# Optimization experiments

Measured on AMD Instinct MI355X. Metric: run time of the kernel, lower is better.

Reference implementation:

```python
import jax, jax.numpy as jnp
import numpy as np

B, NQ, NKV = 4, 1024, 2048
DQ, DC, DI, H = 1024, 1024, 1024, 16
DH = DI // H
EPS = 1e-5


def layer_norm(x, gamma, beta):
    mu = jnp.mean(x, axis=-1, keepdims=True)
    var = jnp.var(x, axis=-1, keepdims=True)
    return (x - mu) * jax.lax.rsqrt(var + EPS) * gamma + beta


def setup_inputs() -> dict:
    key = jax.random.key(0)
    ks = jax.random.split(key, 6)
    s = 0.02
    return {
        "q": jax.random.normal(ks[0], (B, NQ, DQ), jnp.float32),
        "context": jax.random.normal(ks[1], (B, NKV, DC), jnp.float32),
        "Wq": jax.random.normal(ks[2], (DI, DQ), jnp.float32) * s,
        "Wkv": jax.random.normal(ks[3], (2 * DI, DC), jnp.float32) * s,
        "Wproj": jax.random.normal(ks[4], (DQ, DI), jnp.float32) * s,
        "bproj": jnp.zeros((DQ,), jnp.float32),
        "q_gamma": jnp.ones((DQ,), jnp.float32),
        "q_beta": jnp.zeros((DQ,), jnp.float32),
        "c_gamma": jnp.ones((DC,), jnp.float32),
        "c_beta": jnp.zeros((DC,), jnp.float32),
    }


def reference(q, context, Wq, Wkv, Wproj, bproj, q_gamma, q_beta, c_gamma, c_beta):
    scale = DH ** -0.5
    qn = layer_norm(q, q_gamma, q_beta)            # [b, nq, dq]
    cn = layer_norm(context, c_gamma, c_beta)      # [b, nkv, dc]
    qp = qn @ Wq.T                                  # [b, nq, di]
    kv = cn @ Wkv.T                                 # [b, nkv, 2*di]
    k, v = kv[..., :DI], kv[..., DI:]
    qh = qp.reshape(B, NQ, H, DH)
    kh = k.reshape(B, NKV, H, DH)
    vh = v.reshape(B, NKV, H, DH)
    attn = jnp.einsum('bnhd,bmhd->bhnm', qh, kh) * scale   # [b,h,nq,nkv]
    attn = jax.nn.softmax(attn, axis=-1)
    out = jnp.einsum('bhnm,bmhd->bnhd', attn, vh).reshape(B, NQ, DI)
    return out @ Wproj.T + bproj
```

## Files before the change

kernel.cpp:

```cpp
#include <hip/hip_runtime.h>
#include <hip/hip_bf16.h>
#include <stdint.h>

#define B_N 4
#define NQ 1024
#define NKV 2048
#define DI 1024
#define H 16
#define DH 64

using bf16 = __bf16;
typedef bf16 bf16x8 __attribute__((ext_vector_type(8)));
typedef bf16 bf16x4 __attribute__((ext_vector_type(4)));
typedef float f32x4 __attribute__((ext_vector_type(4)));

typedef const __attribute__((address_space(1))) void* gptr_t;
typedef __attribute__((address_space(3))) void* sptr_t;

__global__ __launch_bounds__(256) void cvt_all(const float* __restrict__ Wq,
    const float* __restrict__ Wkv, const float* __restrict__ Wproj,
    bf16* __restrict__ oq, bf16* __restrict__ okv, bf16* __restrict__ op) {
  int i = blockIdx.x * 256 + threadIdx.x;
  const float* src; bf16* dst; int j;
  if (i < 262144)      { src = Wq;    dst = oq;  j = i; }
  else if (i < 786432) { src = Wkv;   dst = okv; j = i - 262144; }
  else                 { src = Wproj; dst = op;  j = i - 786432; }
  float4 v = reinterpret_cast<const float4*>(src)[j];
  bf16x4 o;
  o[0] = (bf16)v.x; o[1] = (bf16)v.y; o[2] = (bf16)v.z; o[3] = (bf16)v.w;
  reinterpret_cast<bf16x4*>(dst)[j] = o;
}

__global__ __launch_bounds__(256) void ln_kernel(const float* __restrict__ q,
    const float* __restrict__ ctx,
    const float* __restrict__ qg, const float* __restrict__ qb,
    const float* __restrict__ cg, const float* __restrict__ cb,
    bf16* __restrict__ qn, bf16* __restrict__ cn) {
  int row = blockIdx.x;
  const float* x; const float* gamma; const float* beta; bf16* out; int r;
  if (row < 4096) { x = q;   gamma = qg; beta = qb; out = qn; r = row; }
  else            { x = ctx; gamma = cg; beta = cb; out = cn; r = row - 4096; }
  int t = threadIdx.x;
  const float4 v = reinterpret_cast<const float4*>(x + (size_t)r * 1024)[t];
  float s = v.x + v.y + v.z + v.w;
  float s2 = v.x*v.x + v.y*v.y + v.z*v.z + v.w*v.w;
#pragma unroll
  for (int m = 1; m < 64; m <<= 1) { s += __shfl_xor(s, m); s2 += __shfl_xor(s2, m); }
  __shared__ float red[8];
  int wid = t >> 6;
  if ((t & 63) == 0) { red[wid] = s; red[wid + 4] = s2; }
  __syncthreads();
  float ts  = red[0] + red[1] + red[2] + red[3];
  float ts2 = red[4] + red[5] + red[6] + red[7];
  float mean = ts * (1.0f / 1024.0f);
  float var  = ts2 * (1.0f / 1024.0f) - mean * mean;
  float rstd = rsqrtf(var + 1e-5f);
  float4 g  = reinterpret_cast<const float4*>(gamma)[t];
  float4 bb = reinterpret_cast<const float4*>(beta)[t];
  bf16x4 o;
  o[0] = (bf16)((v.x - mean) * rstd * g.x + bb.x);
  o[1] = (bf16)((v.y - mean) * rstd * g.y + bb.y);
  o[2] = (bf16)((v.z - mean) * rstd * g.z + bb.z);
  o[3] = (bf16)((v.w - mean) * rstd * g.w + bb.w);
  reinterpret_cast<bf16x4*>(out + (size_t)r * 1024)[t] = o;
}

template<int MODE, int BN>
__device__ __forceinline__ void gemm_body(bf16* lA, bf16* lB,
    const bf16* __restrict__ A, const bf16* __restrict__ Bm,
    void* __restrict__ out0, void* __restrict__ out1,
    const float* __restrict__ bias, int M, int N, int bid) {
  constexpr int K = 1024;
  constexpr int MI = (BN == 128) ? 4 : 2;
  constexpr int NBL = (BN == 128) ? 4 : 2;
  const int nbn = N / BN;
  const int bm = bid / nbn, bn = bid - bm * nbn;
  const int m0 = bm << 7, n0 = bn * BN;
  const int tid = threadIdx.x;
  const int lane = tid & 63, wid = tid >> 6;
  const int rowb = (BN == 128) ? ((wid >> 1) * 64) : (wid * 32);
  const int colb = (BN == 128) ? ((wid & 1) * 64) : 0;
  const int l15 = lane & 15, lg = lane >> 4;

  f32x4 acc[MI][4] = {};

  const bf16* gA[4]; const bf16* gB[NBL];
#pragma unroll
  for (int u = 0; u < 4; ++u) {
    int s = tid + u * 256;
    int row = s >> 3, c8 = (s & 7) ^ (row & 7);
    gA[u] = A + (size_t)(m0 + row) * K + c8 * 8;
  }
#pragma unroll
  for (int u = 0; u < NBL; ++u) {
    int s = tid + u * 256;
    int row = s >> 3, c8 = (s & 7) ^ (row & 7);
    gB[u] = Bm + (size_t)(n0 + row) * K + c8 * 8;
  }

  const int sw = l15 & 7;

  for (int k0 = 0; k0 < K; k0 += 64) {
#pragma unroll
    for (int u = 0; u < 4; ++u)
      __builtin_amdgcn_global_load_lds((gptr_t)(gA[u] + k0), (sptr_t)(lA + (tid + u * 256) * 8), 16, 0, 0);
#pragma unroll
    for (int u = 0; u < NBL; ++u)
      __builtin_amdgcn_global_load_lds((gptr_t)(gB[u] + k0), (sptr_t)(lB + (tid + u * 256) * 8), 16, 0, 0);
    __syncthreads();
#pragma unroll
    for (int ks2 = 0; ks2 < 2; ++ks2) {
      const int soff = ((ks2 * 4 + lg) ^ sw) * 8;
      bf16x8 af[MI], bfr[4];
#pragma unroll
      for (int i = 0; i < MI; ++i)
        af[i]  = *reinterpret_cast<const bf16x8*>(lA + (rowb + i * 16 + l15) * 64 + soff);
#pragma unroll
      for (int j = 0; j < 4; ++j)
        bfr[j] = *reinterpret_cast<const bf16x8*>(lB + (colb + j * 16 + l15) * 64 + soff);
#pragma unroll
      for (int i = 0; i < MI; ++i)
#pragma unroll
        for (int j = 0; j < 4; ++j)
          acc[i][j] = __builtin_amdgcn_mfma_f32_16x16x32_bf16(af[i], bfr[j], acc[i][j], 0, 0, 0);
    }
    __syncthreads();
  }

  const int mB = m0 + rowb + lg * 4;
  const int nB = n0 + colb + l15;
  if constexpr (MODE == 0) {
    bf16* o = reinterpret_cast<bf16*>(out0);
    constexpr float SC = 0.125f * 1.44269504089f;
#pragma unroll
    for (int i = 0; i < MI; ++i)
#pragma unroll
      for (int j = 0; j < 4; ++j)
#pragma unroll
        for (int r = 0; r < 4; ++r)
          o[(size_t)(mB + i * 16 + r) * N + nB + j * 16] = (bf16)(acc[i][j][r] * SC);
  } else if constexpr (MODE == 2) {
    float* o = reinterpret_cast<float*>(out0);
#pragma unroll
    for (int j = 0; j < 4; ++j) {
      float bj = bias[nB + j * 16];
#pragma unroll
      for (int i = 0; i < MI; ++i)
#pragma unroll
        for (int r = 0; r < 4; ++r)
          o[(size_t)(mB + i * 16 + r) * N + nB + j * 16] = acc[i][j][r] + bj;
    }
  } else {
    if (n0 < 1024) {
      bf16* o = reinterpret_cast<bf16*>(out0);
#pragma unroll
      for (int i = 0; i < MI; ++i)
#pragma unroll
        for (int j = 0; j < 4; ++j)
#pragma unroll
          for (int r = 0; r < 4; ++r)
            o[(size_t)(mB + i * 16 + r) * 1024 + nB + j * 16] = (bf16)acc[i][j][r];
    } else {
      bf16* o = reinterpret_cast<bf16*>(out1);
#pragma unroll
      for (int i = 0; i < MI; ++i) {
        int m = mB + i * 16;
        int bb_ = m >> 11, kv = m & 2047;
        int u = kv & 63;
        int c = (u & 32) | ((u & 12) << 1) | ((u & 16) >> 2) | (u & 3);
        int col = (kv & ~63) | c;
#pragma unroll
        for (int j = 0; j < 4; ++j) {
          int nv = nB + j * 16 - 1024;
          bf16x4 pk;
          pk[0] = (bf16)acc[i][j][0]; pk[1] = (bf16)acc[i][j][1];
          pk[2] = (bf16)acc[i][j][2]; pk[3] = (bf16)acc[i][j][3];
          *reinterpret_cast<bf16x4*>(o + ((size_t)(bb_ << 10) + nv) * 2048 + col) = pk;
        }
      }
    }
  }
}

template<int MODE, int BN>
__global__ __launch_bounds__(256) void gemm_bt(const bf16* __restrict__ A,
    const bf16* __restrict__ Bm, void* __restrict__ out0, void* __restrict__ out1,
    const float* __restrict__ bias, int M, int N) {
  __shared__ bf16 lA[128 * 64];
  __shared__ bf16 lB[BN * 64];
  const int cpx = gridDim.x >> 3;
  const int bid = (blockIdx.x & 7) * cpx + (blockIdx.x >> 3);
  gemm_body<MODE, BN>(lA, lB, A, Bm, out0, out1, bias, M, N, bid);
}

__global__ __launch_bounds__(256) void gemm_fused(
    const bf16* __restrict__ qn, const bf16* __restrict__ Wq, void* __restrict__ qpb,
    const bf16* __restrict__ cn, const bf16* __restrict__ Wkv,
    void* __restrict__ kbuf, void* __restrict__ vT) {
  __shared__ bf16 lA[128 * 64];
  __shared__ bf16 lB[128 * 64];
  if (blockIdx.x < 1024) {
    int rb = blockIdx.x;
    int bid = (rb & 7) * 128 + (rb >> 3);
    gemm_body<1, 128>(lA, lB, cn, Wkv, kbuf, vT, nullptr, 8192, 2048, bid);
  } else {
    int rb = blockIdx.x - 1024;
    int bid = (rb & 7) * 32 + (rb >> 3);
    gemm_body<0, 128>(lA, lB, qn, Wq, qpb, nullptr, nullptr, 4096, 1024, bid);
  }
}

__global__ __launch_bounds__(512, 4) void attn_kernel(const bf16* __restrict__ qp,
    const bf16* __restrict__ kk, const bf16* __restrict__ vTp, bf16* __restrict__ out) {
  __shared__ bf16 smem[32768];
  const int pos = blockIdx.x;
  const int idx = pos >> 3;
  const int bh = ((idx >> 3) << 3) | (pos & 7);
  const int qt = idx & 7;
  const int b = bh >> 4, h = bh & 15;
  const int tid = threadIdx.x;
  const int lane = tid & 63, w = tid >> 6;
  const int l15 = lane & 15, lg = lane >> 4;

  const bf16* Qb = qp + (size_t)(b * NQ + qt * 128 + w * 16) * DI + h * DH;
  const bf16* Kb = kk + (size_t)b * NKV * DI + h * DH;
  const bf16* Vb = vTp + (size_t)(b * DI + h * DH) * NKV;

  const int sA = tid, sB = tid + 512;
  const int rKA = ((sA >> 7) << 4) | (sA & 15), cKA = ((sA >> 4) & 7) * 8;
  const int rKB = ((sB >> 7) << 4) | (sB & 15), cKB = ((sB >> 4) & 7) * 8;
  const int rVA = ((sA >> 8) << 4) | (sA & 15), cVA = ((sA >> 6) & 3) * 32 + ((sA >> 4) & 3) * 8;
  const int rVB = ((sB >> 8) << 4) | (sB & 15), cVB = ((sB >> 6) & 3) * 32 + ((sB >> 4) & 3) * 8;
  const bf16* pKA = Kb + (size_t)rKA * DI + cKA;
  const bf16* pKB = Kb + (size_t)rKB * DI + cKB;
  const bf16* pVA = Vb + (size_t)rVA * NKV + cVA;
  const bf16* pVB = Vb + (size_t)rVB * NKV + cVB;

#define STAGE_KV(bufsel, kv)                                                                        \
  do {                                                                                              \
    __builtin_amdgcn_global_load_lds((gptr_t)(pKA + (size_t)(kv) * DI),                             \
                                     (sptr_t)(smem + (bufsel) * 8192 + sA * 8), 16, 0, 0);          \
    __builtin_amdgcn_global_load_lds((gptr_t)(pKB + (size_t)(kv) * DI),                             \
                                     (sptr_t)(smem + (bufsel) * 8192 + sB * 8), 16, 0, 0);          \
    __builtin_amdgcn_global_load_lds((gptr_t)(pVA + (kv)),                                          \
                                     (sptr_t)(smem + 16384 + (bufsel) * 8192 + sA * 8), 16, 0, 0);  \
    __builtin_amdgcn_global_load_lds((gptr_t)(pVB + (kv)),                                          \
                                     (sptr_t)(smem + 16384 + (bufsel) * 8192 + sB * 8), 16, 0, 0);  \
  } while (0)

  bf16x8 qf[2];
#pragma unroll
  for (int ks = 0; ks < 2; ++ks)
    qf[ks] = *reinterpret_cast<const bf16x8*>(Qb + (size_t)l15 * DI + ks * 32 + lg * 8);

  f32x4 o[4] = {};
  float mrun = -1e30f;
  float lpart = 0.0f;

  STAGE_KV(0, 0);
  __syncthreads();
  int cur = 0;

  for (int kv0 = 0; kv0 < NKV; kv0 += 128) {
    const bool notlast = (kv0 + 128 < NKV);
    if (notlast) STAGE_KV(cur ^ 1, kv0 + 128);

    const bf16* Kl = smem + cur * 8192;
    const bf16* Vl = smem + 16384 + cur * 8192;

    f32x4 s[8] = {};
#pragma unroll
    for (int h2 = 0; h2 < 2; ++h2) {
      bf16x8 kf[4][2];
#pragma unroll
      for (int ni = 0; ni < 4; ++ni)
#pragma unroll
        for (int ks = 0; ks < 2; ++ks)
          kf[ni][ks] = *reinterpret_cast<const bf16x8*>(Kl + (((h2 * 4 + ni) * 2 + ks) * 64 + lane) * 8);
      __builtin_amdgcn_s_setprio(1);
#pragma unroll
      for (int ni = 0; ni < 4; ++ni)
#pragma unroll
        for (int ks = 0; ks < 2; ++ks)
          s[h2 * 4 + ni] = __builtin_amdgcn_mfma_f32_16x16x32_bf16(kf[ni][ks], qf[ks], s[h2 * 4 + ni], 0, 0, 0);
      __builtin_amdgcn_s_setprio(0);
    }

    f32x4 mv = s[0];
#pragma unroll
    for (int i = 1; i < 8; ++i) {
      mv[0] = fmaxf(mv[0], s[i][0]); mv[1] = fmaxf(mv[1], s[i][1]);
      mv[2] = fmaxf(mv[2], s[i][2]); mv[3] = fmaxf(mv[3], s[i][3]);
    }
    float pm = fmaxf(fmaxf(mv[0], mv[1]), fmaxf(mv[2], mv[3]));
    pm = fmaxf(pm, __shfl_xor(pm, 16));
    pm = fmaxf(pm, __shfl_xor(pm, 32));

    const bool noresc = __all(pm <= mrun);
    const float mnew = noresc ? mrun : fmaxf(mrun, pm);

    f32x4 sv = {};
#pragma unroll
    for (int i = 0; i < 8; ++i) {
#pragma unroll
      for (int r = 0; r < 4; ++r) {
        s[i][r] = __builtin_amdgcn_exp2f(s[i][r] - mnew);
        sv[r] += s[i][r];
      }
    }
    const float rs_local = (sv[0] + sv[1]) + (sv[2] + sv[3]);

    if (noresc) {
      lpart += rs_local;
    } else {
      float corr = __builtin_amdgcn_exp2f(mrun - mnew);
      lpart = lpart * corr + rs_local;
      mrun = mnew;
      float c0 = __shfl(corr, lg * 4 + 0);
      float c1 = __shfl(corr, lg * 4 + 1);
      float c2 = __shfl(corr, lg * 4 + 2);
      float c3 = __shfl(corr, lg * 4 + 3);
#pragma unroll
      for (int dt = 0; dt < 4; ++dt) {
        o[dt][0] *= c0; o[dt][1] *= c1; o[dt][2] *= c2; o[dt][3] *= c3;
      }
    }

    bf16x8 pa[4];
#pragma unroll
    for (int h2 = 0; h2 < 2; ++h2)
#pragma unroll
      for (int k2p = 0; k2p < 2; ++k2p)
#pragma unroll
        for (int jj = 0; jj < 4; ++jj) {
          pa[h2 * 2 + k2p][jj]     = (bf16)s[h2 * 4 + k2p * 2 + 0][jj];
          pa[h2 * 2 + k2p][4 + jj] = (bf16)s[h2 * 4 + k2p * 2 + 1][jj];
        }

    __builtin_amdgcn_s_setprio(1);
#pragma unroll
    for (int k2 = 0; k2 < 4; ++k2) {
      bf16x8 vf[4];
#pragma unroll
      for (int dt = 0; dt < 4; ++dt)
        vf[dt] = *reinterpret_cast<const bf16x8*>(Vl + ((dt * 4 + k2) * 64 + lane) * 8);
#pragma unroll
      for (int dt = 0; dt < 4; ++dt)
        o[dt] = __builtin_amdgcn_mfma_f32_16x16x32_bf16(pa[k2], vf[dt], o[dt], 0, 0, 0);
    }
    __builtin_amdgcn_s_setprio(0);

    if (notlast) __syncthreads();
    cur ^= 1;
  }
#undef STAGE_KV

  float lsum = lpart;
  lsum += __shfl_xor(lsum, 16);
  lsum += __shfl_xor(lsum, 32);
  const float inv = 1.0f / lsum;
  const float iv0 = __shfl(inv, lg * 4 + 0);
  const float iv1 = __shfl(inv, lg * 4 + 1);
  const float iv2 = __shfl(inv, lg * 4 + 2);
  const float iv3 = __shfl(inv, lg * 4 + 3);

  bf16* Ob = out + (size_t)(b * NQ + qt * 128 + w * 16) * DI + h * DH;
#pragma unroll
  for (int dt = 0; dt < 4; ++dt) {
    Ob[(size_t)(lg * 4 + 0) * DI + dt * 16 + l15] = (bf16)(o[dt][0] * iv0);
    Ob[(size_t)(lg * 4 + 1) * DI + dt * 16 + l15] = (bf16)(o[dt][1] * iv1);
    Ob[(size_t)(lg * 4 + 2) * DI + dt * 16 + l15] = (bf16)(o[dt][2] * iv2);
    Ob[(size_t)(lg * 4 + 3) * DI + dt * 16 + l15] = (bf16)(o[dt][3] * iv3);
  }
}

extern "C" void kernel_launch(void* const* d_in, const int* in_sizes, int n_in,
                              void* d_out, int out_size, void* d_ws, size_t ws_size,
                              hipStream_t stream) {
  const float* q     = (const float*)d_in[0];
  const float* ctx   = (const float*)d_in[1];
  const float* Wq    = (const float*)d_in[2];
  const float* Wkv   = (const float*)d_in[3];
  const float* Wproj = (const float*)d_in[4];
  const float* bproj = (const float*)d_in[5];
  const float* qg    = (const float*)d_in[6];
  const float* qb    = (const float*)d_in[7];
  const float* cg    = (const float*)d_in[8];
  const float* cb    = (const float*)d_in[9];

  char* ws = (char*)d_ws;
  bf16* qn    = (bf16*)(ws);
  bf16* cn    = (bf16*)(ws + ( 8ull << 20));
  bf16* Wq_b  = (bf16*)(ws + (24ull << 20));
  bf16* Wkv_b = (bf16*)(ws + (26ull << 20));
  bf16* Wp_b  = (bf16*)(ws + (30ull << 20));
  bf16* qpb   = (bf16*)(ws + (32ull << 20));
  bf16* kbuf  = (bf16*)(ws + (40ull << 20));
  bf16* vT    = (bf16*)(ws + (56ull << 20));
  bf16* aout  = (bf16*)(ws + (72ull << 20));

  cvt_all<<<4096, 256, 0, stream>>>(Wq, Wkv, Wproj, Wq_b, Wkv_b, Wp_b);
  ln_kernel<<<12288, 256, 0, stream>>>(q, ctx, qg, qb, cg, cb, qn, cn);

  gemm_fused<<<1280, 256, 0, stream>>>(qn, Wq_b, qpb, cn, Wkv_b, kbuf, vT);

  attn_kernel<<<512, 512, 0, stream>>>(qpb, kbuf, vT, aout);

  gemm_bt<2, 64><<<512, 256, 0, stream>>>(aout, Wp_b, d_out, nullptr, bproj, 4096, 1024);
}
```

Measured before the change: 142.5 us.

## Double-buffer GEMM LDS tiles with K=32 stages and MFMA priority boost

The shared GEMM body now loads 32-wide K slices into two LDS buffers, prefetching the next stage while MFMAs run on the current one. Previously it used a single 64-wide buffer with a load-then-compute barrier pattern. The XOR swizzle is adjusted for the 32-element row stride, and s_setprio is raised around the MFMA block. This hides global-to-LDS latency, at the cost of twice as many barrier-synchronised iterations with smaller per-stage work.

```diff
diff --git a/kernel.cpp b/kernel.cpp
--- a/kernel.cpp
+++ b/kernel.cpp
@@ -66,13 +66,15 @@
 }
 
 template<int MODE, int BN>
-__device__ __forceinline__ void gemm_body(bf16* lA, bf16* lB,
+__device__ __forceinline__ void gemm2_body(bf16* lA, bf16* lB,
     const bf16* __restrict__ A, const bf16* __restrict__ Bm,
     void* __restrict__ out0, void* __restrict__ out1,
-    const float* __restrict__ bias, int M, int N, int bid) {
+    const float* __restrict__ bias, int N, int bid) {
   constexpr int K = 1024;
-  constexpr int MI = (BN == 128) ? 4 : 2;
-  constexpr int NBL = (BN == 128) ? 4 : 2;
+  constexpr int MI  = (BN == 128) ? 4 : 2;
+  constexpr int NBL = (BN == 128) ? 2 : 1;
+  constexpr int AE = 128 * 32;
+  constexpr int BE = BN * 32;
   const int nbn = N / BN;
   const int bm = bid / nbn, bn = bid - bm * nbn;
   const int m0 = bm << 7, n0 = bn * BN;
@@ -84,48 +86,59 @@
 
   f32x4 acc[MI][4] = {};
 
-  const bf16* gA[4]; const bf16* gB[NBL];
-#pragma unroll
-  for (int u = 0; u < 4; ++u) {
+  const bf16* gA[2]; const bf16* gB[NBL];
+#pragma unroll
+  for (int u = 0; u < 2; ++u) {
     int s = tid + u * 256;
-    int row = s >> 3, c8 = (s & 7) ^ (row & 7);
-    gA[u] = A + (size_t)(m0 + row) * K + c8 * 8;
+    gA[u] = A + (size_t)(m0 + (s >> 2)) * K + (((s & 3) ^ ((s >> 3) & 3)) << 3);
   }
 #pragma unroll
   for (int u = 0; u < NBL; ++u) {
     int s = tid + u * 256;
-    int row = s >> 3, c8 = (s & 7) ^ (row & 7);
-    gB[u] = Bm + (size_t)(n0 + row) * K + c8 * 8;
-  }
-
-  const int sw = l15 & 7;
-
-  for (int k0 = 0; k0 < K; k0 += 64) {
-#pragma unroll
-    for (int u = 0; u < 4; ++u)
-      __builtin_amdgcn_global_load_lds((gptr_t)(gA[u] + k0), (sptr_t)(lA + (tid + u * 256) * 8), 16, 0, 0);
-#pragma unroll
-    for (int u = 0; u < NBL; ++u)
-      __builtin_amdgcn_global_load_lds((gptr_t)(gB[u] + k0), (sptr_t)(lB + (tid + u * 256) * 8), 16, 0, 0);
+    gB[u] = Bm + (size_t)(n0 + (s >> 2)) * K + (((s & 3) ^ ((s >> 3) & 3)) << 3);
+  }
+
+#define G2STAGE(buf, k0)                                                                             \
+  do {                                                                                               \
+    _Pragma("unroll")                                                                                \
+    for (int u = 0; u < 2; ++u)                                                                      \
+      __builtin_amdgcn_global_load_lds((gptr_t)(gA[u] + (k0)),                                       \
+          (sptr_t)(lA + (buf) * AE + (tid + u * 256) * 8), 16, 0, 0);                                \
+    _Pragma("unroll")                                                                                \
+    for (int u = 0; u < NBL; ++u)                                                                    \
+      __builtin_amdgcn_global_load_lds((gptr_t)(gB[u] + (k0)),                                       \
+          (sptr_t)(lB + (buf) * BE + (tid + u * 256) * 8), 16, 0, 0);                                \
+  } while (0)
+
+  G2STAGE(0, 0);
+  __syncthreads();
+  int cur = 0;
+
+  const int soff = (lg ^ ((l15 >> 1) & 3)) * 8;
+
+  for (int kt = 0; kt < 32; ++kt) {
+    if (kt < 31) G2STAGE(cur ^ 1, (kt + 1) * 32);
+
+    const bf16* lAc = lA + cur * AE;
+    const bf16* lBc = lB + cur * BE;
+    bf16x8 af[MI], bfr[4];
+#pragma unroll
+    for (int i = 0; i < MI; ++i)
+      af[i]  = *reinterpret_cast<const bf16x8*>(lAc + (rowb + i * 16 + l15) * 32 + soff);
+#pragma unroll
+    for (int j = 0; j < 4; ++j)
+      bfr[j] = *reinterpret_cast<const bf16x8*>(lBc + (colb + j * 16 + l15) * 32 + soff);
+    __builtin_amdgcn_s_setprio(1);
+#pragma unroll
+    for (int i = 0; i < MI; ++i)
+#pragma unroll
+      for (int j = 0; j < 4; ++j)
+        acc[i][j] = __builtin_amdgcn_mfma_f32_16x16x32_bf16(af[i], bfr[j], acc[i][j], 0, 0, 0);
+    __builtin_amdgcn_s_setprio(0);
     __syncthreads();
-#pragma unroll
-    for (int ks2 = 0; ks2 < 2; ++ks2) {
-      const int soff = ((ks2 * 4 + lg) ^ sw) * 8;
-      bf16x8 af[MI], bfr[4];
-#pragma unroll
-      for (int i = 0; i < MI; ++i)
-        af[i]  = *reinterpret_cast<const bf16x8*>(lA + (rowb + i * 16 + l15) * 64 + soff);
-#pragma unroll
-      for (int j = 0; j < 4; ++j)
-        bfr[j] = *reinterpret_cast<const bf16x8*>(lB + (colb + j * 16 + l15) * 64 + soff);
-#pragma unroll
-      for (int i = 0; i < MI; ++i)
-#pragma unroll
-        for (int j = 0; j < 4; ++j)
-          acc[i][j] = __builtin_amdgcn_mfma_f32_16x16x32_bf16(af[i], bfr[j], acc[i][j], 0, 0, 0);
-    }
-    __syncthreads();
-  }
+    cur ^= 1;
+  }
+#undef G2STAGE
 
   const int mB = m0 + rowb + lg * 4;
   const int nB = n0 + colb + l15;
@@ -182,32 +195,31 @@
   }
 }
 
-template<int MODE, int BN>
-__global__ __launch_bounds__(256) void gemm_bt(const bf16* __restrict__ A,
-    const bf16* __restrict__ Bm, void* __restrict__ out0, void* __restrict__ out1,
-    const float* __restrict__ bias, int M, int N) {
-  __shared__ bf16 lA[128 * 64];
-  __shared__ bf16 lB[BN * 64];
-  const int cpx = gridDim.x >> 3;
-  const int bid = (blockIdx.x & 7) * cpx + (blockIdx.x >> 3);
-  gemm_body<MODE, BN>(lA, lB, A, Bm, out0, out1, bias, M, N, bid);
-}
-
 __global__ __launch_bounds__(256) void gemm_fused(
     const bf16* __restrict__ qn, const bf16* __restrict__ Wq, void* __restrict__ qpb,
     const bf16* __restrict__ cn, const bf16* __restrict__ Wkv,
     void* __restrict__ kbuf, void* __restrict__ vT) {
-  __shared__ bf16 lA[128 * 64];
-  __shared__ bf16 lB[128 * 64];
+  __shared__ bf16 lA[2 * 128 * 32];
+  __shared__ bf16 lB[2 * 128 * 32];
   if (blockIdx.x < 1024) {
     int rb = blockIdx.x;
     int bid = (rb & 7) * 128 + (rb >> 3);
-    gemm_body<1, 128>(lA, lB, cn, Wkv, kbuf, vT, nullptr, 8192, 2048, bid);
+    gemm2_body<1, 128>(lA, lB, cn, Wkv, kbuf, vT, nullptr, 2048, bid);
   } else {
     int rb = blockIdx.x - 1024;
     int bid = (rb & 7) * 32 + (rb >> 3);
-    gemm_body<0, 128>(lA, lB, qn, Wq, qpb, nullptr, nullptr, 4096, 1024, bid);
-  }
+    gemm2_body<0, 128>(lA, lB, qn, Wq, qpb, nullptr, nullptr, 1024, bid);
+  }
+}
+
+__global__ __launch_bounds__(256) void gemm_proj(const bf16* __restrict__ A,
+    const bf16* __restrict__ Bm, void* __restrict__ out0,
+    const float* __restrict__ bias) {
+  __shared__ bf16 lA[2 * 128 * 32];
+  __shared__ bf16 lB[2 * 64 * 32];
+  const int cpx = gridDim.x >> 3;
+  const int bid = (blockIdx.x & 7) * cpx + (blockIdx.x >> 3);
+  gemm2_body<2, 64>(lA, lB, A, Bm, out0, nullptr, bias, 1024, bid);
 }
 
 __global__ __launch_bounds__(512, 4) void attn_kernel(const bf16* __restrict__ qp,
@@ -406,5 +418,5 @@
 
   attn_kernel<<<512, 512, 0, stream>>>(qpb, kbuf, vT, aout);
 
-  gemm_bt<2, 64><<<512, 256, 0, stream>>>(aout, Wp_b, d_out, nullptr, bproj, 4096, 1024);
-}
+  gemm_proj<<<512, 256, 0, stream>>>(aout, Wp_b, d_out, bproj);
+}
```

Result: slower. 158.8 us (+11.4%).
